# Optimization experiments

Hardware: AMD Instinct MI355X
Metric: run time of the kernel (lower is better)

## Reference

```python
import jax, jax.numpy as jnp
import numpy as np

N_NODES = 50000
N_EDGES = 800000
IN_DIM = 128
HID_DIM = 128
OUT_DIM = 128


def setup_inputs() -> dict:
    key = jax.random.key(0)
    k = jax.random.split(key, 8)
    x = jax.random.normal(k[0], (N_NODES, IN_DIM), dtype=jnp.float32)
    edge_index = jax.random.randint(k[1], (2, N_EDGES), 0, N_NODES, dtype=jnp.int64)
    edge_weight = jax.random.uniform(k[2], (N_EDGES,), dtype=jnp.float32)
    # GCNConv params: weight [in, out] (glorot-ish), bias [out]
    W1 = jax.random.normal(k[3], (IN_DIM, HID_DIM), dtype=jnp.float32) / np.sqrt(IN_DIM)
    b1 = jnp.zeros((HID_DIM,), dtype=jnp.float32)
    W2 = jax.random.normal(k[4], (HID_DIM, OUT_DIM), dtype=jnp.float32) / np.sqrt(HID_DIM)
    b2 = jnp.zeros((OUT_DIM,), dtype=jnp.float32)
    return {"x": x, "edge_index": edge_index, "edge_weight": edge_weight,
            "W1": W1, "b1": b1, "W2": W2, "b2": b2}


def gcn_conv(x, W, b, src, dst, ew, n_nodes):
    """PyG GCNConv: add self-loops (weight 1), symmetric D^-1/2 (A+I) D^-1/2 norm."""
    h = x @ W  # [N, out]
    deg = jax.ops.segment_sum(ew, dst, num_segments=n_nodes) + 1.0  # +1 for self loop
    dis = jnp.where(deg > 0, jax.lax.rsqrt(deg), 0.0)  # deg^{-1/2}
    norm = dis[src] * ew * dis[dst]  # [E]
    msg = h[src] * norm[:, None]  # gather + weight -> [E, out]
    agg = jax.ops.segment_sum(msg, dst, num_segments=n_nodes)
    # self-loop contribution: norm_ii = dis[i] * 1 * dis[i]
    agg = agg + h * (dis * dis)[:, None]
    return agg + b


def reference(x, edge_index, edge_weight, W1, b1, W2, b2):
    src, dst = edge_index[0], edge_index[1]
    n = x.shape[0]
    h = gcn_conv(x, W1, b1, src, dst, edge_weight, n)
    h = jax.nn.relu(h)
    out = gcn_conv(h, W2, b2, src, dst, edge_weight, n)
    return out
```

## Files before the change

### kernel.cpp

```cpp
#include <hip/hip_runtime.h>

#define NDIM 128

typedef __attribute__((ext_vector_type(8))) short bf16x8;
typedef __attribute__((ext_vector_type(4))) float floatx4;

__device__ __forceinline__ float bflo(unsigned v){ return __uint_as_float(v << 16); }
__device__ __forceinline__ float bfhi(unsigned v){ return __uint_as_float(v & 0xffff0000u); }
__device__ __forceinline__ unsigned f2bf(float f){
  unsigned u = __float_as_uint(f);
  return (u + 0x7fffu + ((u >> 16) & 1u)) >> 16;
}

__global__ void k_init(unsigned long long* pk, int n){
  int i = blockIdx.x * blockDim.x + threadIdx.x;
  if (i < n) pk[i] = 0ULL;
}

__global__ void k_deg(const int* __restrict__ ei, const float* __restrict__ ew,
                      unsigned long long* pk, int E){
  int e = blockIdx.x * blockDim.x + threadIdx.x;
  if (e >= E) return;
  int d = ei[E + e];
  unsigned fx = (unsigned)__float2uint_rn(ew[e] * 1048576.0f);
  atomicAdd(&pk[d], (1ULL << 44) | (unsigned long long)fx);
}

__global__ __launch_bounds__(1024) void k_scan1(const unsigned long long* __restrict__ pk,
                                                int* __restrict__ off,
                                                int* __restrict__ bsum, int n){
  __shared__ int wsum[16];
  int t = threadIdx.x;
  int i = blockIdx.x * 1024 + t;
  int c = (i < n) ? (int)(pk[i] >> 44) : 0;
  int lane = t & 63, w = t >> 6;
  int v = c;
  #pragma unroll
  for (int d = 1; d < 64; d <<= 1){ int u = __shfl_up(v, d); if (lane >= d) v += u; }
  if (lane == 63) wsum[w] = v;
  __syncthreads();
  if (w == 0){
    int sv = (lane < 16) ? wsum[lane] : 0;
    #pragma unroll
    for (int d = 1; d < 16; d <<= 1){ int u = __shfl_up(sv, d); if (lane >= d) sv += u; }
    if (lane < 16) wsum[lane] = sv;
  }
  __syncthreads();
  int base = (w > 0) ? wsum[w - 1] : 0;
  if (i < n) off[i] = base + v - c;
  if (t == 1023) bsum[blockIdx.x] = wsum[15];
}

__global__ void k_scan2(int* bsum, int nb){
  int lane = threadIdx.x & 63;
  int c = (lane < nb) ? bsum[lane] : 0;
  int v = c;
  #pragma unroll
  for (int d = 1; d < 64; d <<= 1){ int u = __shfl_up(v, d); if (lane >= d) v += u; }
  if (lane < nb) bsum[lane] = v - c;
}

__global__ __launch_bounds__(1024) void k_scan3(int* __restrict__ off, int* __restrict__ cur,
                                                const int* __restrict__ bsum,
                                                const unsigned long long* __restrict__ pk,
                                                float* __restrict__ dis, int n, int E){
  int i = blockIdx.x * 1024 + threadIdx.x;
  if (i == 0) off[n] = E;
  if (i >= n) return;
  int o = off[i] + bsum[blockIdx.x];
  off[i] = o; cur[i] = o;
  float deg = 1.0f + (float)(pk[i] & ((1ULL << 44) - 1)) * (1.0f / 1048576.0f);
  dis[i] = rsqrtf(deg);
}

__global__ void k_place(const int* __restrict__ ei, const float* __restrict__ ew,
                        const float* __restrict__ dis, int* cur, unsigned* edges, int E){
  int e = blockIdx.x * blockDim.x + threadIdx.x;
  if (e >= E) return;
  int s = ei[e], d = ei[E + e];
  int p = atomicAdd(&cur[d], 1);
  edges[p] = (f2bf(dis[s] * ew[e] * dis[d]) << 16) | (unsigned)s;
}

__global__ void k_wprep(const float* __restrict__ W, unsigned short* __restrict__ Wp){
  int t = blockIdx.x * 256 + threadIdx.x;
  int k = t >> 7, n = t & 127;
  int kt = k >> 5, kq = (k >> 3) & 3, j = k & 7;
  int Lb = kq * 16 + (n & 15);
  Wp[(((kt * 8 + (n >> 4)) * 64) + Lb) * 8 + j] = (unsigned short)f2bf(W[t]);
}

template<int XF32>
__global__ __launch_bounds__(256) void k_gemm_mfma(const void* __restrict__ Xv,
                                                   const unsigned short* __restrict__ Wp,
                                                   unsigned short* __restrict__ Hout,
                                                   int ntiles){
  __shared__ unsigned short Wb[4 * 8 * 64 * 8];
  int tid = threadIdx.x;
  for (int t = tid; t < 2048; t += 256)
    ((uint4*)Wb)[t] = ((const uint4*)Wp)[t];
  __syncthreads();

  int w = tid >> 6, L = tid & 63;
  int m = L & 15, q = L >> 4;
  for (int tile = blockIdx.x * 4 + w; tile < ntiles; tile += gridDim.x * 4){
    size_t row = (size_t)tile * 16 + m;
    floatx4 acc[8] = {};
    #pragma unroll
    for (int kt = 0; kt < 4; ++kt){
      bf16x8 a;
      if (XF32){
        const float* xp = (const float*)Xv + row * NDIM + kt * 32 + q * 8;
        float4 a0 = *(const float4*)xp;
        float4 a1 = *(const float4*)(xp + 4);
        unsigned short* as = (unsigned short*)&a;
        as[0] = f2bf(a0.x); as[1] = f2bf(a0.y); as[2] = f2bf(a0.z); as[3] = f2bf(a0.w);
        as[4] = f2bf(a1.x); as[5] = f2bf(a1.y); as[6] = f2bf(a1.z); as[7] = f2bf(a1.w);
      } else {
        a = *(const bf16x8*)((const unsigned short*)Xv + row * NDIM + kt * 32 + q * 8);
      }
      #pragma unroll
      for (int ct = 0; ct < 8; ++ct){
        bf16x8 b = *(const bf16x8*)&Wb[((kt * 8 + ct) * 64 + L) * 8];
        acc[ct] = __builtin_amdgcn_mfma_f32_16x16x32_bf16(a, b, acc[ct], 0, 0, 0);
      }
    }
    #pragma unroll
    for (int ct = 0; ct < 8; ++ct){
      #pragma unroll
      for (int r = 0; r < 4; ++r){
        size_t orow = (size_t)tile * 16 + q * 4 + r;
        Hout[orow * NDIM + ct * 16 + m] = (unsigned short)f2bf(acc[ct][r]);
      }
    }
  }
}

template<int OUT_F32>
__global__ __launch_bounds__(256) void k_agg(const unsigned short* __restrict__ H,
                                             const int* __restrict__ off,
                                             const unsigned* __restrict__ edges,
                                             const float* __restrict__ dis,
                                             const float* __restrict__ bias,
                                             void* __restrict__ out,
                                             int n, int do_relu){
  int g = threadIdx.x >> 6, L = threadIdx.x & 63;
  int i = blockIdx.x * 4 + g;
  if (i >= n) return;
  float di = dis[i];
  float2 bv = ((const float2*)bias)[L];
  unsigned hv = ((const unsigned*)(H + (size_t)i * NDIM))[L];
  float acc0 = bv.x + bflo(hv) * di * di;
  float acc1 = bv.y + bfhi(hv) * di * di;
  int p = off[i], p1 = off[i + 1];
  while (p + 8 <= p1){
    unsigned e[8], h[8];
    #pragma unroll
    for (int j = 0; j < 8; ++j) e[j] = edges[p + j];
    #pragma unroll
    for (int j = 0; j < 8; ++j)
      h[j] = ((const unsigned*)(H + (size_t)(e[j] & 0xFFFF) * NDIM))[L];
    #pragma unroll
    for (int j = 0; j < 8; ++j){
      float w = bfhi(e[j]);
      acc0 = fmaf(bflo(h[j]), w, acc0);
      acc1 = fmaf(bfhi(h[j]), w, acc1);
    }
    p += 8;
  }
  for (; p < p1; ++p){
    unsigned e = edges[p];
    unsigned h2 = ((const unsigned*)(H + (size_t)(e & 0xFFFF) * NDIM))[L];
    float w = bfhi(e);
    acc0 = fmaf(bflo(h2), w, acc0);
    acc1 = fmaf(bfhi(h2), w, acc1);
  }
  if (do_relu){ acc0 = fmaxf(acc0, 0.f); acc1 = fmaxf(acc1, 0.f); }
  if (OUT_F32){
    ((float2*)((float*)out + (size_t)i * NDIM))[L] = make_float2(acc0, acc1);
  } else {
    ((unsigned*)((unsigned short*)out + (size_t)i * NDIM))[L] = (f2bf(acc1) << 16) | f2bf(acc0);
  }
}

extern "C" void kernel_launch(void* const* d_in, const int* in_sizes, int n_in,
                              void* d_out, int out_size, void* d_ws, size_t ws_size,
                              hipStream_t stream){
  const float* x  = (const float*)d_in[0];
  const int*   ei = (const int*)  d_in[1];
  const float* ew = (const float*)d_in[2];
  const float* W1 = (const float*)d_in[3];
  const float* b1 = (const float*)d_in[4];
  const float* W2 = (const float*)d_in[5];
  const float* b2 = (const float*)d_in[6];
  float* out = (float*)d_out;
  int N = in_sizes[0] / NDIM;
  int E = in_sizes[2];
  int nb = (N + 1023) / 1024;
  int ntiles = N / 16;

  char* p = (char*)d_ws;
  auto alloc = [&](size_t b) -> char* { char* r = p; p += (b + 255) & ~(size_t)255; return r; };
  unsigned long long* pk = (unsigned long long*)alloc((size_t)N * 8);
  float*    dis   = (float*)   alloc((size_t)N * 4);
  int*      cur   = (int*)     alloc((size_t)N * 4);
  int*      off   = (int*)     alloc((size_t)(N + 1) * 4);
  int*      bsum  = (int*)     alloc((size_t)64 * 4);
  unsigned short* Wp1 = (unsigned short*)alloc(NDIM * NDIM * 2);
  unsigned short* Wp2 = (unsigned short*)alloc(NDIM * NDIM * 2);
  unsigned* edges = (unsigned*)alloc((size_t)E * 4);
  unsigned short* R = (unsigned short*)alloc((size_t)N * NDIM * 2);
  unsigned short* H1 = (unsigned short*)d_out;

  k_init <<<(N + 255) / 256, 256, 0, stream>>>(pk, N);
  k_deg  <<<(E + 255) / 256, 256, 0, stream>>>(ei, ew, pk, E);
  k_scan1<<<nb, 1024, 0, stream>>>(pk, off, bsum, N);
  k_scan2<<<1, 64, 0, stream>>>(bsum, nb);
  k_scan3<<<nb, 1024, 0, stream>>>(off, cur, bsum, pk, dis, N, E);
  k_place<<<(E + 255) / 256, 256, 0, stream>>>(ei, ew, dis, cur, edges, E);
  k_wprep<<<64, 256, 0, stream>>>(W1, Wp1);
  k_wprep<<<64, 256, 0, stream>>>(W2, Wp2);

  k_gemm_mfma<1><<<512, 256, 0, stream>>>(x, Wp1, H1, ntiles);
  k_agg<0> <<<(N + 3) / 4, 256, 0, stream>>>(H1, off, edges, dis, b1, R, N, 1);
  k_gemm_mfma<0><<<512, 256, 0, stream>>>(R, Wp2, R, ntiles);
  k_agg<1> <<<(N + 3) / 4, 256, 0, stream>>>(R, off, edges, dis, b2, out, N, 0);
}
```

Before: 267.3 us.

## Fuse layer-1 aggregation with layer-2 GEMM via LDS tile staging

Layer-1 aggregation and the second GEMM are merged into one kernel. Each wave aggregates 16 node rows into an LDS tile, applies ReLU, then runs MFMA against W2 held in LDS, so the intermediate activation no longer makes a round trip through global memory. Also replaces the init kernel with a memset, merges the two weight-prep launches, unrolls the edge loop to 16 and changes the GEMM grid size. The risk is that each wave now walks 16 rows serially, which cuts per-row parallelism and latency hiding in the gather-heavy aggregation.

```diff
diff --git a/kernel.cpp b/kernel.cpp
--- a/kernel.cpp
+++ b/kernel.cpp
@@ -10,11 +10,6 @@
 __device__ __forceinline__ unsigned f2bf(float f){
   unsigned u = __float_as_uint(f);
   return (u + 0x7fffu + ((u >> 16) & 1u)) >> 16;
-}
-
-__global__ void k_init(unsigned long long* pk, int n){
-  int i = blockIdx.x * blockDim.x + threadIdx.x;
-  if (i < n) pk[i] = 0ULL;
 }
 
 __global__ void k_deg(const int* __restrict__ ei, const float* __restrict__ ew,
@@ -82,12 +77,16 @@
   edges[p] = (f2bf(dis[s] * ew[e] * dis[d]) << 16) | (unsigned)s;
 }
 
-__global__ void k_wprep(const float* __restrict__ W, unsigned short* __restrict__ Wp){
+__global__ void k_wprep2(const float* __restrict__ W1, unsigned short* __restrict__ Wp1,
+                         const float* __restrict__ W2, unsigned short* __restrict__ Wp2){
   int t = blockIdx.x * 256 + threadIdx.x;
-  int k = t >> 7, n = t & 127;
+  const float* W = (t < 16384) ? W1 : W2;
+  unsigned short* Wp = (t < 16384) ? Wp1 : Wp2;
+  int tt = t & 16383;
+  int k = tt >> 7, n = tt & 127;
   int kt = k >> 5, kq = (k >> 3) & 3, j = k & 7;
   int Lb = kq * 16 + (n & 15);
-  Wp[(((kt * 8 + (n >> 4)) * 64) + Lb) * 8 + j] = (unsigned short)f2bf(W[t]);
+  Wp[(((kt * 8 + (n >> 4)) * 64) + Lb) * 8 + j] = (unsigned short)f2bf(W[tt]);
 }
 
 template<int XF32>
@@ -95,7 +94,7 @@
                                                    const unsigned short* __restrict__ Wp,
                                                    unsigned short* __restrict__ Hout,
                                                    int ntiles){
-  __shared__ unsigned short Wb[4 * 8 * 64 * 8];
+  __shared__ unsigned short Wb[2048 * 8];
   int tid = threadIdx.x;
   for (int t = tid; t < 2048; t += 256)
     ((uint4*)Wb)[t] = ((const uint4*)Wp)[t];
@@ -136,14 +135,105 @@
   }
 }
 
-template<int OUT_F32>
-__global__ __launch_bounds__(256) void k_agg(const unsigned short* __restrict__ H,
-                                             const int* __restrict__ off,
-                                             const unsigned* __restrict__ edges,
-                                             const float* __restrict__ dis,
-                                             const float* __restrict__ bias,
-                                             void* __restrict__ out,
-                                             int n, int do_relu){
+__device__ __forceinline__ void edge_accum(const unsigned short* __restrict__ H,
+                                           const unsigned* __restrict__ edges,
+                                           int p, int p1, int L,
+                                           float& acc0, float& acc1){
+  while (p + 16 <= p1){
+    unsigned e[16], h[16];
+    #pragma unroll
+    for (int j = 0; j < 16; ++j) e[j] = edges[p + j];
+    #pragma unroll
+    for (int j = 0; j < 16; ++j)
+      h[j] = ((const unsigned*)(H + (size_t)(e[j] & 0xFFFF) * NDIM))[L];
+    #pragma unroll
+    for (int j = 0; j < 16; ++j){
+      float w = bfhi(e[j]);
+      acc0 = fmaf(bflo(h[j]), w, acc0);
+      acc1 = fmaf(bfhi(h[j]), w, acc1);
+    }
+    p += 16;
+  }
+  if (p + 8 <= p1){
+    unsigned e[8], h[8];
+    #pragma unroll
+    for (int j = 0; j < 8; ++j) e[j] = edges[p + j];
+    #pragma unroll
+    for (int j = 0; j < 8; ++j)
+      h[j] = ((const unsigned*)(H + (size_t)(e[j] & 0xFFFF) * NDIM))[L];
+    #pragma unroll
+    for (int j = 0; j < 8; ++j){
+      float w = bfhi(e[j]);
+      acc0 = fmaf(bflo(h[j]), w, acc0);
+      acc1 = fmaf(bfhi(h[j]), w, acc1);
+    }
+    p += 8;
+  }
+  for (; p < p1; ++p){
+    unsigned e = edges[p];
+    unsigned h2 = ((const unsigned*)(H + (size_t)(e & 0xFFFF) * NDIM))[L];
+    float w = bfhi(e);
+    acc0 = fmaf(bflo(h2), w, acc0);
+    acc1 = fmaf(bfhi(h2), w, acc1);
+  }
+}
+
+__global__ __launch_bounds__(256) void k_aggemm(const unsigned short* __restrict__ H,
+                                                const int* __restrict__ off,
+                                                const unsigned* __restrict__ edges,
+                                                const float* __restrict__ dis,
+                                                const float* __restrict__ bias,
+                                                const unsigned short* __restrict__ Wp,
+                                                unsigned short* __restrict__ Hout,
+                                                int ntiles){
+  __shared__ unsigned short Wb[2048 * 8];
+  __shared__ unsigned short At[4][16 * 136];
+  int tid = threadIdx.x;
+  for (int t = tid; t < 2048; t += 256)
+    ((uint4*)Wb)[t] = ((const uint4*)Wp)[t];
+  __syncthreads();
+
+  int w = tid >> 6, L = tid & 63;
+  int m = L & 15, q = L >> 4;
+  for (int tile = blockIdx.x * 4 + w; tile < ntiles; tile += gridDim.x * 4){
+    for (int r = 0; r < 16; ++r){
+      int i = tile * 16 + r;
+      float di = dis[i];
+      float2 bv = ((const float2*)bias)[L];
+      unsigned hv = ((const unsigned*)(H + (size_t)i * NDIM))[L];
+      float acc0 = bv.x + bflo(hv) * di * di;
+      float acc1 = bv.y + bfhi(hv) * di * di;
+      edge_accum(H, edges, off[i], off[i + 1], L, acc0, acc1);
+      acc0 = fmaxf(acc0, 0.f); acc1 = fmaxf(acc1, 0.f);
+      *(unsigned*)&At[w][r * 136 + L * 2] = (f2bf(acc1) << 16) | f2bf(acc0);
+    }
+    floatx4 acc[8] = {};
+    #pragma unroll
+    for (int kt = 0; kt < 4; ++kt){
+      bf16x8 a = *(const bf16x8*)&At[w][m * 136 + kt * 32 + q * 8];
+      #pragma unroll
+      for (int ct = 0; ct < 8; ++ct){
+        bf16x8 b = *(const bf16x8*)&Wb[((kt * 8 + ct) * 64 + L) * 8];
+        acc[ct] = __builtin_amdgcn_mfma_f32_16x16x32_bf16(a, b, acc[ct], 0, 0, 0);
+      }
+    }
+    #pragma unroll
+    for (int ct = 0; ct < 8; ++ct){
+      #pragma unroll
+      for (int r = 0; r < 4; ++r){
+        size_t orow = (size_t)tile * 16 + q * 4 + r;
+        Hout[orow * NDIM + ct * 16 + m] = (unsigned short)f2bf(acc[ct][r]);
+      }
+    }
+  }
+}
+
+__global__ __launch_bounds__(256) void k_agg_f32(const unsigned short* __restrict__ H,
+                                                 const int* __restrict__ off,
+                                                 const unsigned* __restrict__ edges,
+                                                 const float* __restrict__ dis,
+                                                 const float* __restrict__ bias,
+                                                 float* __restrict__ out, int n){
   int g = threadIdx.x >> 6, L = threadIdx.x & 63;
   int i = blockIdx.x * 4 + g;
   if (i >= n) return;
@@ -152,35 +242,8 @@
   unsigned hv = ((const unsigned*)(H + (size_t)i * NDIM))[L];
   float acc0 = bv.x + bflo(hv) * di * di;
   float acc1 = bv.y + bfhi(hv) * di * di;
-  int p = off[i], p1 = off[i + 1];
-  while (p + 8 <= p1){
-    unsigned e[8], h[8];
-    #pragma unroll
-    for (int j = 0; j < 8; ++j) e[j] = edges[p + j];
-    #pragma unroll
-    for (int j = 0; j < 8; ++j)
-      h[j] = ((const unsigned*)(H + (size_t)(e[j] & 0xFFFF) * NDIM))[L];
-    #pragma unroll
-    for (int j = 0; j < 8; ++j){
-      float w = bfhi(e[j]);
-      acc0 = fmaf(bflo(h[j]), w, acc0);
-      acc1 = fmaf(bfhi(h[j]), w, acc1);
-    }
-    p += 8;
-  }
-  for (; p < p1; ++p){
-    unsigned e = edges[p];
-    unsigned h2 = ((const unsigned*)(H + (size_t)(e & 0xFFFF) * NDIM))[L];
-    float w = bfhi(e);
-    acc0 = fmaf(bflo(h2), w, acc0);
-    acc1 = fmaf(bfhi(h2), w, acc1);
-  }
-  if (do_relu){ acc0 = fmaxf(acc0, 0.f); acc1 = fmaxf(acc1, 0.f); }
-  if (OUT_F32){
-    ((float2*)((float*)out + (size_t)i * NDIM))[L] = make_float2(acc0, acc1);
-  } else {
-    ((unsigned*)((unsigned short*)out + (size_t)i * NDIM))[L] = (f2bf(acc1) << 16) | f2bf(acc0);
-  }
+  edge_accum(H, edges, off[i], off[i + 1], L, acc0, acc1);
+  ((float2*)(out + (size_t)i * NDIM))[L] = make_float2(acc0, acc1);
 }
 
 extern "C" void kernel_launch(void* const* d_in, const int* in_sizes, int n_in,
@@ -212,17 +275,15 @@
   unsigned short* R = (unsigned short*)alloc((size_t)N * NDIM * 2);
   unsigned short* H1 = (unsigned short*)d_out;
 
-  k_init <<<(N + 255) / 256, 256, 0, stream>>>(pk, N);
-  k_deg  <<<(E + 255) / 256, 256, 0, stream>>>(ei, ew, pk, E);
-  k_scan1<<<nb, 1024, 0, stream>>>(pk, off, bsum, N);
-  k_scan2<<<1, 64, 0, stream>>>(bsum, nb);
-  k_scan3<<<nb, 1024, 0, stream>>>(off, cur, bsum, pk, dis, N, E);
-  k_place<<<(E + 255) / 256, 256, 0, stream>>>(ei, ew, dis, cur, edges, E);
-  k_wprep<<<64, 256, 0, stream>>>(W1, Wp1);
-  k_wprep<<<64, 256, 0, stream>>>(W2, Wp2);
-
-  k_gemm_mfma<1><<<512, 256, 0, stream>>>(x, Wp1, H1, ntiles);
-  k_agg<0> <<<(N + 3) / 4, 256, 0, stream>>>(H1, off, edges, dis, b1, R, N, 1);
-  k_gemm_mfma<0><<<512, 256, 0, stream>>>(R, Wp2, R, ntiles);
-  k_agg<1> <<<(N + 3) / 4, 256, 0, stream>>>(R, off, edges, dis, b2, out, N, 0);
-}
+  hipMemsetAsync(pk, 0, (size_t)N * 8, stream);
+  k_deg   <<<(E + 255) / 256, 256, 0, stream>>>(ei, ew, pk, E);
+  k_scan1 <<<nb, 1024, 0, stream>>>(pk, off, bsum, N);
+  k_scan2 <<<1, 64, 0, stream>>>(bsum, nb);
+  k_scan3 <<<nb, 1024, 0, stream>>>(off, cur, bsum, pk, dis, N, E);
+  k_place <<<(E + 255) / 256, 256, 0, stream>>>(ei, ew, dis, cur, edges, E);
+  k_wprep2<<<128, 256, 0, stream>>>(W1, Wp1, W2, Wp2);
+
+  k_gemm_mfma<1><<<782, 256, 0, stream>>>(x, Wp1, H1, ntiles);
+  k_aggemm      <<<782, 256, 0, stream>>>(H1, off, edges, dis, b1, Wp2, R, ntiles);
+  k_agg_f32     <<<(N + 3) / 4, 256, 0, stream>>>(R, off, edges, dis, b2, out, N);
+}
```

New measurement: 328.8 us. +23.0%, slower.
